# Optimization experiments

Hardware: AMD Instinct MI355X
Metric: run time of the kernel (lower is better)

The kernel has to match this reference:

```python
import jax, jax.numpy as jnp
import numpy as np

B, S, D, H, E, K, F = 8, 2048, 1024, 16, 32, 8, 1024
HD = D // H
EPS = 1e-5


def _ln(x, scale, bias):
    m = jnp.mean(x, axis=-1, keepdims=True)
    v = jnp.mean(jnp.square(x - m), axis=-1, keepdims=True)
    return (x - m) * jax.lax.rsqrt(v + EPS) * scale + bias


def setup_inputs() -> dict:
    key = jax.random.key(0)
    ks = jax.random.split(key, 14)
    w = lambda k, shp: jax.random.normal(k, shp, jnp.float32) * 0.02
    return {
        "hidden_states": jax.random.normal(ks[0], (B, S, D), jnp.float32),
        "ln1_scale": jnp.ones((D,), jnp.float32),
        "ln1_bias": jnp.zeros((D,), jnp.float32),
        "wq": w(ks[1], (D, D)), "bq": jnp.zeros((D,), jnp.float32),
        "wk": w(ks[2], (D, D)), "bk": jnp.zeros((D,), jnp.float32),
        "wv": w(ks[3], (D, D)), "bv": jnp.zeros((D,), jnp.float32),
        "ln2_scale": jnp.ones((D,), jnp.float32),
        "ln2_bias": jnp.zeros((D,), jnp.float32),
        "router_w": w(ks[4], (D, E)), "router_b": jnp.zeros((E,), jnp.float32),
        "w1": w(ks[5], (E, D, F)), "b1": jnp.zeros((E, F), jnp.float32),
        "w2": w(ks[6], (E, F, D)), "b2": jnp.zeros((E, D), jnp.float32),
    }


def reference(hidden_states, ln1_scale, ln1_bias, wq, bq, wk, bk, wv, bv,
              ln2_scale, ln2_bias, router_w, router_b, w1, b1, w2, b2):
    # --- attention sub-block (faithful to source: scores are [B,S,H,H]) ---
    x = _ln(hidden_states, ln1_scale, ln1_bias)
    q = (x @ wq + bq).reshape(B, S, H, HD)
    k = (x @ wk + bk).reshape(B, S, H, HD)
    v = (x @ wv + bv).reshape(B, S, H, HD)
    scores = jnp.einsum('bshd,bsgd->bshg', q, k) / np.sqrt(HD).astype(np.float32)
    probs = jax.nn.softmax(scores, axis=-1)
    ctx = jnp.einsum('bshg,bsgd->bshd', probs, v).reshape(B, S, D)
    h1 = hidden_states + ctx
    # --- MoE sub-block: per-token top-K of E experts ---
    x2 = _ln(h1, ln2_scale, ln2_bias)
    router_probs = jax.nn.softmax(x2 @ router_w + router_b, axis=-1)  # [B,S,E]
    top_w, top_i = jax.lax.top_k(router_probs, K)
    top_w = top_w / jnp.sum(top_w, axis=-1, keepdims=True)
    # dense per-token gate over experts (zero for unselected)
    gates = jnp.sum(jax.nn.one_hot(top_i, E, dtype=x2.dtype) * top_w[..., None], axis=-2)  # [B,S,E]
    moe = jnp.zeros_like(x2)
    for e in range(E):  # fixed small expert set; unrolled under jit
        h = jax.nn.gelu(x2 @ w1[e] + b1[e], approximate=False)
        moe = moe + gates[..., e:e + 1] * (h @ w2[e] + b2[e])
    return h1 + moe
```

## Files before the change

kernel.cpp:

```cpp
#include <hip/hip_runtime.h>
#include <hip/hip_bf16.h>
#include <stdint.h>

#define TOK 16384
#define DD  1024
#define NE  32

typedef unsigned short u16;
typedef __attribute__((ext_vector_type(8))) short short8;
typedef __attribute__((ext_vector_type(4))) float f32x4;

__device__ __forceinline__ u16 f2bf(float f) {
  unsigned int u = __float_as_uint(f);
  u += 0x7fffu + ((u >> 16) & 1u);
  return (u16)(u >> 16);
}
__device__ __forceinline__ float bf2f(u16 h) {
  return __uint_as_float(((unsigned int)h) << 16);
}
__device__ __forceinline__ void gload16(const void* g, void* l) {
  __builtin_amdgcn_global_load_lds((const __attribute__((address_space(1))) void*)g,
                                   (__attribute__((address_space(3))) void*)l, 16, 0, 0);
}

__global__ __launch_bounds__(256) void k_transpose(const float* __restrict__ src,
                                                   u16* __restrict__ dst, int R, int C) {
  __shared__ float tile[32][33];
  size_t mb = (size_t)blockIdx.z * R * C;
  int c0 = blockIdx.x * 32, r0 = blockIdx.y * 32;
  int tx = threadIdx.x, ty = threadIdx.y;
#pragma unroll
  for (int i = 0; i < 4; i++)
    tile[ty + i * 8][tx] = src[mb + (size_t)(r0 + ty + i * 8) * C + c0 + tx];
  __syncthreads();
#pragma unroll
  for (int i = 0; i < 4; i++) {
    float v = tile[tx][ty + i * 8];
    dst[mb + (size_t)(c0 + ty + i * 8) * R + r0 + tx] = f2bf(v);
  }
}

__global__ __launch_bounds__(256) void k_transpose_split(const float* __restrict__ src,
                                                         u16* __restrict__ hi,
                                                         u16* __restrict__ lo, int R, int C) {
  __shared__ float tile[32][33];
  int c0 = blockIdx.x * 32, r0 = blockIdx.y * 32;
  int tx = threadIdx.x, ty = threadIdx.y;
#pragma unroll
  for (int i = 0; i < 4; i++)
    tile[ty + i * 8][tx] = src[(size_t)(r0 + ty + i * 8) * C + c0 + tx];
  __syncthreads();
#pragma unroll
  for (int i = 0; i < 4; i++) {
    float v = tile[tx][ty + i * 8];
    u16 h = f2bf(v);
    u16 l = f2bf(v - bf2f(h));
    size_t idx = (size_t)(c0 + ty + i * 8) * R + r0 + tx;
    hi[idx] = h;
    lo[idx] = l;
  }
}

__global__ __launch_bounds__(256) void k_ln1(const float* __restrict__ x,
                                             const float* __restrict__ sc,
                                             const float* __restrict__ bi,
                                             u16* __restrict__ ohi, u16* __restrict__ olo) {
  __shared__ float red[10];
  int t = blockIdx.x, tid = threadIdx.x;
  size_t base = (size_t)t * DD + tid * 4;
  float4 v = *(const float4*)(x + base);
  float s1 = v.x + v.y + v.z + v.w;
  float s2 = v.x * v.x + v.y * v.y + v.z * v.z + v.w * v.w;
  for (int o = 1; o < 64; o <<= 1) { s1 += __shfl_xor(s1, o, 64); s2 += __shfl_xor(s2, o, 64); }
  int wid = tid >> 6;
  if ((tid & 63) == 0) { red[wid * 2] = s1; red[wid * 2 + 1] = s2; }
  __syncthreads();
  if (tid == 0) {
    float a = 0, b = 0;
    for (int i = 0; i < 4; i++) { a += red[i * 2]; b += red[i * 2 + 1]; }
    float mean = a * (1.f / DD);
    float var = b * (1.f / DD) - mean * mean;
    red[8] = mean; red[9] = rsqrtf(var + 1e-5f);
  }
  __syncthreads();
  float mean = red[8], rs = red[9];
  int e0 = tid * 4;
  float xv[4] = {v.x, v.y, v.z, v.w};
  ushort4 oh, ol;
  u16* ph = (u16*)&oh; u16* pl = (u16*)&ol;
#pragma unroll
  for (int i = 0; i < 4; i++) {
    float f = (xv[i] - mean) * rs * sc[e0 + i] + bi[e0 + i];
    u16 h = f2bf(f);
    ph[i] = h;
    pl[i] = f2bf(f - bf2f(h));
  }
  *(ushort4*)(ohi + base) = oh;
  *(ushort4*)(olo + base) = ol;
}

__global__ __launch_bounds__(256) void k_attn(
    const float* __restrict__ hidden, const float* __restrict__ qb,
    const float* __restrict__ kb, const float* __restrict__ vb,
    const float* __restrict__ ln2s, const float* __restrict__ ln2b,
    const float* __restrict__ rw, const float* __restrict__ rb,
    float* __restrict__ out, u16* __restrict__ x2b, float* __restrict__ gates) {
  __shared__ float qs[16][68], ks[16][68], vs[16][68];
  __shared__ float probs[16][17];
  __shared__ float x2s[1024];
  __shared__ float red[12];
  __shared__ float part[8][32];
  __shared__ float logits[32];
  int t = blockIdx.x, tid = threadIdx.x;
  size_t base = (size_t)t * DD + tid * 4;
  int hh = tid >> 4, dd = (tid & 15) * 4;
  {
    float4 q4 = *(const float4*)(qb + base);
    float4 k4 = *(const float4*)(kb + base);
    float4 v4 = *(const float4*)(vb + base);
    qs[hh][dd + 0] = q4.x; qs[hh][dd + 1] = q4.y; qs[hh][dd + 2] = q4.z; qs[hh][dd + 3] = q4.w;
    ks[hh][dd + 0] = k4.x; ks[hh][dd + 1] = k4.y; ks[hh][dd + 2] = k4.z; ks[hh][dd + 3] = k4.w;
    vs[hh][dd + 0] = v4.x; vs[hh][dd + 1] = v4.y; vs[hh][dd + 2] = v4.z; vs[hh][dd + 3] = v4.w;
  }
  __syncthreads();
  {
    int g = tid & 15;
    float s = 0.f;
#pragma unroll
    for (int d = 0; d < 64; d++) s += qs[hh][d] * ks[g][d];
    s *= 0.125f;
    float mx = s;
    for (int o = 1; o < 16; o <<= 1) mx = fmaxf(mx, __shfl_xor(mx, o, 16));
    float p = __expf(s - mx);
    float sm = p;
    for (int o = 1; o < 16; o <<= 1) sm += __shfl_xor(sm, o, 16);
    probs[hh][g] = p / sm;
  }
  __syncthreads();
  float c0 = 0, c1 = 0, c2 = 0, c3 = 0;
#pragma unroll
  for (int g = 0; g < 16; g++) {
    float pw = probs[hh][g];
    c0 += pw * vs[g][dd + 0]; c1 += pw * vs[g][dd + 1];
    c2 += pw * vs[g][dd + 2]; c3 += pw * vs[g][dd + 3];
  }
  float4 hv = *(const float4*)(hidden + base);
  float h0 = hv.x + c0, h1 = hv.y + c1, h2 = hv.z + c2, h3 = hv.w + c3;
  { float4 o4; o4.x = h0; o4.y = h1; o4.z = h2; o4.w = h3; *(float4*)(out + base) = o4; }
  float s1 = h0 + h1 + h2 + h3;
  float s2 = h0 * h0 + h1 * h1 + h2 * h2 + h3 * h3;
  for (int o = 1; o < 64; o <<= 1) { s1 += __shfl_xor(s1, o, 64); s2 += __shfl_xor(s2, o, 64); }
  int wid = tid >> 6;
  if ((tid & 63) == 0) { red[wid * 2] = s1; red[wid * 2 + 1] = s2; }
  __syncthreads();
  if (tid == 0) {
    float a = 0, b = 0;
    for (int i = 0; i < 4; i++) { a += red[i * 2]; b += red[i * 2 + 1]; }
    float mean = a * (1.f / DD);
    float var = b * (1.f / DD) - mean * mean;
    red[8] = mean; red[9] = rsqrtf(var + 1e-5f);
  }
  __syncthreads();
  float mean = red[8], rs = red[9];
  int e0 = tid * 4;
  float x0 = (h0 - mean) * rs * ln2s[e0 + 0] + ln2b[e0 + 0];
  float x1 = (h1 - mean) * rs * ln2s[e0 + 1] + ln2b[e0 + 1];
  float x2 = (h2 - mean) * rs * ln2s[e0 + 2] + ln2b[e0 + 2];
  float x3 = (h3 - mean) * rs * ln2s[e0 + 3] + ln2b[e0 + 3];
  ushort4 xo; xo.x = f2bf(x0); xo.y = f2bf(x1); xo.z = f2bf(x2); xo.w = f2bf(x3);
  *(ushort4*)(x2b + base) = xo;
  x2s[e0 + 0] = x0; x2s[e0 + 1] = x1; x2s[e0 + 2] = x2; x2s[e0 + 3] = x3;
  __syncthreads();
  {
    int e = tid & 31, seg = tid >> 5;
    const float* rwp = rw + (size_t)(seg * 128) * NE + e;
    float acc = 0.f;
#pragma unroll 8
    for (int i = 0; i < 128; i++) acc += x2s[seg * 128 + i] * rwp[(size_t)i * NE];
    part[seg][e] = acc;
  }
  __syncthreads();
  if (tid < 32) {
    float l = rb[tid];
#pragma unroll
    for (int s = 0; s < 8; s++) l += part[s][tid];
    logits[tid] = l;
    float mx = l;
    for (int o = 1; o < 32; o <<= 1) mx = fmaxf(mx, __shfl_xor(mx, o, 32));
    float p = __expf(l - mx);
    float sm = p;
    for (int o = 1; o < 32; o <<= 1) sm += __shfl_xor(sm, o, 32);
    p /= sm;
    bool sel = false;
#pragma unroll
    for (int rsel = 0; rsel < 8; rsel++) {
      float bv = sel ? -1.f : p;
      int bi_ = tid;
      for (int o = 1; o < 32; o <<= 1) {
        float ov = __shfl_xor(bv, o, 32);
        int oi = __shfl_xor(bi_, o, 32);
        if (ov > bv || (ov == bv && oi < bi_)) { bv = ov; bi_ = oi; }
      }
      if (tid == bi_) sel = true;
    }
    float wsel = sel ? p : 0.f;
    float ts = wsel;
    for (int o = 1; o < 32; o <<= 1) ts += __shfl_xor(ts, o, 32);
    gates[(size_t)t * 32 + tid] = sel ? (p / ts) : 0.f;
  }
}

__global__ void k_zero32(int* p) { int i = threadIdx.x; if (i < 32) p[i] = 0; }

__global__ void k_listbuild(const float* __restrict__ gates, int* __restrict__ counts,
                            int* __restrict__ lists) {
  int t = blockIdx.x * 256 + threadIdx.x;
  for (int e = 0; e < NE; e++) {
    if (gates[(size_t)t * 32 + e] > 0.f) {
      int pos = atomicAdd(&counts[e], 1);
      lists[(size_t)e * TOK + pos] = t;
    }
  }
}

__global__ void k_scan(const int* __restrict__ counts, int* __restrict__ segoff) {
  if (threadIdx.x == 0) { int s = 0; for (int e = 0; e < NE; e++) { segoff[e] = s; s += counts[e]; } }
}

__global__ __launch_bounds__(256) void k_gemm_p(
    const u16* __restrict__ Ahi, const u16* __restrict__ Alo,
    const u16* __restrict__ qkvT,
    const float* __restrict__ bq, const float* __restrict__ bk, const float* __restrict__ bv,
    float* __restrict__ Cbase) {
  constexpr int KD = 1024;
  __shared__ alignas(16) u16 As[2][2][128 * 32];
  __shared__ alignas(16) u16 Bs[2][2][128 * 32];
  const int tid = threadIdx.x;
  const int w = tid >> 6, lane = tid & 63;
  const int bm = blockIdx.x, bn = blockIdx.y, z = blockIdx.z;
  const u16* Bhi = qkvT + (size_t)z * (2u * KD * KD);
  const u16* Blo = Bhi + (size_t)KD * KD;
  const float* bias = (z == 0) ? bq : (z == 1) ? bk : bv;
  float* C = Cbase + (size_t)z * TOK * KD;

  int rowA[2], qA[2], rowB[2];
#pragma unroll
  for (int i = 0; i < 2; i++) {
    int c = (w * 2 + i) * 64 + lane;
    int r = c >> 2;
    qA[i] = c & 3;
    rowB[i] = bn * 128 + r;
    rowA[i] = bm * 128 + r;
  }

  auto stage = [&](int buf, int k0) {
#pragma unroll
    for (int i = 0; i < 2; i++) {
      size_t ga = (size_t)rowA[i] * KD + k0 + qA[i] * 8;
      size_t gb = (size_t)rowB[i] * KD + k0 + qA[i] * 8;
      int lo_off = (w * 2 + i) * 1024;
      gload16(Ahi + ga, (char*)&As[buf][0][0] + lo_off);
      gload16(Alo + ga, (char*)&As[buf][1][0] + lo_off);
      gload16(Bhi + gb, (char*)&Bs[buf][0][0] + lo_off);
      gload16(Blo + gb, (char*)&Bs[buf][1][0] + lo_off);
    }
  };

  f32x4 acc[4][4];
#pragma unroll
  for (int m = 0; m < 4; m++)
#pragma unroll
    for (int n = 0; n < 4; n++) acc[m][n] = (f32x4)0.f;

  const int wr = (w >> 1) * 64, wc = (w & 1) * 64;
  const int la = lane & 15, lk = (lane >> 4) * 8;

  stage(0, 0);
  __syncthreads();
  for (int kt = 0; kt < 32; kt++) {
    const int cur = kt & 1;
    if (kt + 1 < 32) stage(cur ^ 1, (kt + 1) * 32);
    short8 ah[4], al[4], bh[4], bl[4];
#pragma unroll
    for (int m = 0; m < 4; m++) {
      ah[m] = *(const short8*)&As[cur][0][(wr + m * 16 + la) * 32 + lk];
      al[m] = *(const short8*)&As[cur][1][(wr + m * 16 + la) * 32 + lk];
    }
#pragma unroll
    for (int n = 0; n < 4; n++) {
      bh[n] = *(const short8*)&Bs[cur][0][(wc + n * 16 + la) * 32 + lk];
      bl[n] = *(const short8*)&Bs[cur][1][(wc + n * 16 + la) * 32 + lk];
    }
#pragma unroll
    for (int m = 0; m < 4; m++)
#pragma unroll
      for (int n = 0; n < 4; n++) {
        acc[m][n] = __builtin_amdgcn_mfma_f32_16x16x32_bf16(ah[m], bh[n], acc[m][n], 0, 0, 0);
        acc[m][n] = __builtin_amdgcn_mfma_f32_16x16x32_bf16(ah[m], bl[n], acc[m][n], 0, 0, 0);
        acc[m][n] = __builtin_amdgcn_mfma_f32_16x16x32_bf16(al[m], bh[n], acc[m][n], 0, 0, 0);
      }
    __syncthreads();
  }

  const int rl4 = (lane >> 4) * 4;
#pragma unroll
  for (int m = 0; m < 4; m++) {
#pragma unroll
    for (int n = 0; n < 4; n++) {
      const int col = bn * 128 + wc + n * 16 + la;
      const float bvv = bias[col];
      f32x4 a4 = acc[m][n];
#pragma unroll
      for (int r = 0; r < 4; r++) {
        const int grow = bm * 128 + wr + m * 16 + rl4 + r;
        C[(size_t)grow * KD + col] = a4[r] + bvv;
      }
    }
  }
}

template <int MODE>
__global__ __launch_bounds__(256) void k_gemm(
    const u16* __restrict__ A, const u16* __restrict__ BT, const float* __restrict__ bias,
    u16* __restrict__ Cb, float* __restrict__ Cf,
    const int* __restrict__ lists, const int* __restrict__ counts,
    const float* __restrict__ gatesp, const int* __restrict__ segoff) {
  constexpr int KD = 1024;
  __shared__ alignas(16) u16 As[2][128 * 32];
  __shared__ alignas(16) u16 Bs[2][128 * 32];

  int e = (int)blockIdx.z;
  int count = counts[e];
  if ((int)blockIdx.x * 128 >= count) return;
  const int* list = lists + (size_t)e * TOK;
  int so = segoff[e];
  const u16* Bp = BT + (size_t)e * (KD * KD);
  const float* bp = bias + (size_t)e * KD;

  const int tid = threadIdx.x;
  const int w = tid >> 6, lane = tid & 63;
  const int bm = blockIdx.x, bn = blockIdx.y;

  int rowA[2], qA[2], rowB[2];
#pragma unroll
  for (int i = 0; i < 2; i++) {
    int c = (w * 2 + i) * 64 + lane;
    int r = c >> 2;
    qA[i] = c & 3;
    rowB[i] = bn * 128 + r;
    int rr = bm * 128 + r;
    if constexpr (MODE == 1) rowA[i] = (rr < count) ? list[rr] : 0;
    else                     rowA[i] = so + ((rr < count) ? rr : 0);
  }

  auto stage = [&](int buf, int k0) {
#pragma unroll
    for (int i = 0; i < 2; i++) {
      gload16(A + (size_t)rowA[i] * KD + k0 + qA[i] * 8,
              (char*)&As[buf][0] + (w * 2 + i) * 1024);
      gload16(Bp + (size_t)rowB[i] * KD + k0 + qA[i] * 8,
              (char*)&Bs[buf][0] + (w * 2 + i) * 1024);
    }
  };

  f32x4 acc[4][4];
#pragma unroll
  for (int m = 0; m < 4; m++)
#pragma unroll
    for (int n = 0; n < 4; n++) acc[m][n] = (f32x4)0.f;

  const int wr = (w >> 1) * 64, wc = (w & 1) * 64;
  const int la = lane & 15, lk = (lane >> 4) * 8;

  stage(0, 0);
  __syncthreads();
#pragma unroll 2
  for (int kt = 0; kt < 32; kt++) {
    const int cur = kt & 1;
    if (kt + 1 < 32) stage(cur ^ 1, (kt + 1) * 32);
    short8 af[4], bf8[4];
#pragma unroll
    for (int m = 0; m < 4; m++)
      af[m] = *(const short8*)&As[cur][(wr + m * 16 + la) * 32 + lk];
#pragma unroll
    for (int n = 0; n < 4; n++)
      bf8[n] = *(const short8*)&Bs[cur][(wc + n * 16 + la) * 32 + lk];
#pragma unroll
    for (int m = 0; m < 4; m++)
#pragma unroll
      for (int n = 0; n < 4; n++)
        acc[m][n] = __builtin_amdgcn_mfma_f32_16x16x32_bf16(af[m], bf8[n], acc[m][n], 0, 0, 0);
    __syncthreads();
  }

  const int rl4 = (lane >> 4) * 4;
#pragma unroll
  for (int m = 0; m < 4; m++) {
#pragma unroll
    for (int n = 0; n < 4; n++) {
      const int col = bn * 128 + wc + n * 16 + la;
      const float bvv = bp[col];
      f32x4 a4 = acc[m][n];
#pragma unroll
      for (int r = 0; r < 4; r++) {
        const int grow = bm * 128 + wr + m * 16 + rl4 + r;
        float v = a4[r] + bvv;
        if constexpr (MODE == 1) {
          if (grow < count) {
            float gx = 0.5f * v * (1.0f + erff(v * 0.70710678f));
            Cb[(size_t)(so + grow) * KD + col] = f2bf(gx);
          }
        } else {
          if (grow < count) {
            const int tok = list[grow];
            const float gw = gatesp[(size_t)tok * 32 + e];
            atomicAdd(Cf + (size_t)tok * KD + col, v * gw);
          }
        }
      }
    }
  }
}

extern "C" void kernel_launch(void* const* d_in, const int* in_sizes, int n_in,
                              void* d_out, int out_size, void* d_ws, size_t ws_size,
                              hipStream_t stream) {
  (void)in_sizes; (void)n_in; (void)out_size; (void)ws_size;
  const float* hidden = (const float*)d_in[0];
  const float* ln1s = (const float*)d_in[1];
  const float* ln1b = (const float*)d_in[2];
  const float* wq = (const float*)d_in[3];
  const float* bq = (const float*)d_in[4];
  const float* wk = (const float*)d_in[5];
  const float* bk = (const float*)d_in[6];
  const float* wv = (const float*)d_in[7];
  const float* bv = (const float*)d_in[8];
  const float* ln2s = (const float*)d_in[9];
  const float* ln2b = (const float*)d_in[10];
  const float* rw = (const float*)d_in[11];
  const float* rb = (const float*)d_in[12];
  const float* w1 = (const float*)d_in[13];
  const float* b1 = (const float*)d_in[14];
  const float* w2 = (const float*)d_in[15];
  const float* b2 = (const float*)d_in[16];
  float* out = (float*)d_out;

  char* wsp = (char*)d_ws;
  size_t off = 0;
  auto alloc = [&](size_t b) -> void* {
    void* p = wsp + off;
    off += (b + 255) & ~(size_t)255;
    return p;
  };
  u16* wT = (u16*)alloc((size_t)NE * DD * DD * 2);
  u16* x_hi = (u16*)alloc((size_t)TOK * DD * 2);
  float* gates = (float*)alloc((size_t)TOK * NE * 4);
  int* counts = (int*)alloc(NE * 4);
  int* segoff = (int*)alloc((NE + 1) * 4);
  int* lists = (int*)alloc((size_t)NE * TOK * 4);
  char* pool = (char*)alloc((size_t)TOK * 8 * DD * 2);
  u16* qkvT = (u16*)pool;
  u16* x_lo = (u16*)(pool + 12u * 1024 * 1024);
  float* qkv = (float*)(pool + 44u * 1024 * 1024);
  float* qbuf = qkv;
  float* kbuf = qkv + (size_t)TOK * DD;
  float* vbuf = qkv + 2 * (size_t)TOK * DD;
  u16* h_buf = (u16*)pool;

  dim3 tb32(32, 8, 1);
  k_zero32<<<1, 64, 0, stream>>>(counts);
  k_transpose_split<<<dim3(32, 32, 1), tb32, 0, stream>>>(wq, qkvT, qkvT + (size_t)DD * DD, DD, DD);
  k_transpose_split<<<dim3(32, 32, 1), tb32, 0, stream>>>(wk, qkvT + 2 * (size_t)DD * DD, qkvT + 3 * (size_t)DD * DD, DD, DD);
  k_transpose_split<<<dim3(32, 32, 1), tb32, 0, stream>>>(wv, qkvT + 4 * (size_t)DD * DD, qkvT + 5 * (size_t)DD * DD, DD, DD);
  k_transpose<<<dim3(32, 32, NE), tb32, 0, stream>>>(w1, wT, DD, DD);
  k_ln1<<<TOK, 256, 0, stream>>>(hidden, ln1s, ln1b, x_hi, x_lo);
  k_gemm_p<<<dim3(128, 8, 3), 256, 0, stream>>>(x_hi, x_lo, qkvT, bq, bk, bv, qkv);
  k_attn<<<TOK, 256, 0, stream>>>(hidden, qbuf, kbuf, vbuf, ln2s, ln2b, rw, rb, out, x_hi, gates);
  k_listbuild<<<TOK / 256, 256, 0, stream>>>(gates, counts, lists);
  k_scan<<<1, 32, 0, stream>>>(counts, segoff);
  k_gemm<1><<<dim3(128, 8, NE), 256, 0, stream>>>(x_hi, wT, b1, h_buf, nullptr, lists, counts, nullptr, segoff);
  k_transpose<<<dim3(32, 32, NE), tb32, 0, stream>>>(w2, wT, DD, DD);
  k_gemm<2><<<dim3(128, 8, NE), 256, 0, stream>>>(h_buf, wT, b2, nullptr, out, lists, counts, gates, segoff);
}
```

Before: 2.532 ms.

## Replace atomic scatter-add in second MoE GEMM with bf16 staging and gather

```diff
diff --git a/kernel.cpp b/kernel.cpp
--- a/kernel.cpp
+++ b/kernel.cpp
@@ -110,7 +110,6 @@
   __shared__ float x2s[1024];
   __shared__ float red[12];
   __shared__ float part[8][32];
-  __shared__ float logits[32];
   int t = blockIdx.x, tid = threadIdx.x;
   size_t base = (size_t)t * DD + tid * 4;
   int hh = tid >> 4, dd = (tid & 15) * 4;
@@ -184,7 +183,6 @@
     float l = rb[tid];
 #pragma unroll
     for (int s = 0; s < 8; s++) l += part[s][tid];
-    logits[tid] = l;
     float mx = l;
     for (int o = 1; o < 32; o <<= 1) mx = fmaxf(mx, __shfl_xor(mx, o, 32));
     float p = __expf(l - mx);
@@ -213,12 +211,18 @@
 __global__ void k_zero32(int* p) { int i = threadIdx.x; if (i < 32) p[i] = 0; }
 
 __global__ void k_listbuild(const float* __restrict__ gates, int* __restrict__ counts,
-                            int* __restrict__ lists) {
+                            int* __restrict__ lists, int* __restrict__ slots,
+                            float* __restrict__ gsel) {
   int t = blockIdx.x * 256 + threadIdx.x;
+  int j = 0;
   for (int e = 0; e < NE; e++) {
-    if (gates[(size_t)t * 32 + e] > 0.f) {
+    float g = gates[(size_t)t * 32 + e];
+    if (g > 0.f && j < 8) {
       int pos = atomicAdd(&counts[e], 1);
       lists[(size_t)e * TOK + pos] = t;
+      slots[t * 8 + j] = (e << 14) | pos;
+      gsel[t * 8 + j] = g;
+      j++;
     }
   }
 }
@@ -319,12 +323,10 @@
   }
 }
 
-template <int MODE>
-__global__ __launch_bounds__(256) void k_gemm(
+__global__ __launch_bounds__(256) void k_gemm1(
     const u16* __restrict__ A, const u16* __restrict__ BT, const float* __restrict__ bias,
-    u16* __restrict__ Cb, float* __restrict__ Cf,
-    const int* __restrict__ lists, const int* __restrict__ counts,
-    const float* __restrict__ gatesp, const int* __restrict__ segoff) {
+    u16* __restrict__ Cb, const int* __restrict__ lists, const int* __restrict__ counts,
+    const int* __restrict__ segoff) {
   constexpr int KD = 1024;
   __shared__ alignas(16) u16 As[2][128 * 32];
   __shared__ alignas(16) u16 Bs[2][128 * 32];
@@ -349,8 +351,7 @@
     qA[i] = c & 3;
     rowB[i] = bn * 128 + r;
     int rr = bm * 128 + r;
-    if constexpr (MODE == 1) rowA[i] = (rr < count) ? list[rr] : 0;
-    else                     rowA[i] = so + ((rr < count) ? rr : 0);
+    rowA[i] = (rr < count) ? list[rr] : 0;
   }
 
   auto stage = [&](int buf, int k0) {
@@ -404,28 +405,132 @@
 #pragma unroll
       for (int r = 0; r < 4; r++) {
         const int grow = bm * 128 + wr + m * 16 + rl4 + r;
-        float v = a4[r] + bvv;
-        if constexpr (MODE == 1) {
-          if (grow < count) {
-            float gx = 0.5f * v * (1.0f + erff(v * 0.70710678f));
-            Cb[(size_t)(so + grow) * KD + col] = f2bf(gx);
-          }
-        } else {
-          if (grow < count) {
-            const int tok = list[grow];
-            const float gw = gatesp[(size_t)tok * 32 + e];
-            atomicAdd(Cf + (size_t)tok * KD + col, v * gw);
-          }
+        if (grow < count) {
+          float v = a4[r] + bvv;
+          float gx = 0.5f * v * (1.0f + erff(v * 0.70710678f));
+          Cb[(size_t)(so + grow) * KD + col] = f2bf(gx);
         }
       }
     }
   }
+}
+
+__global__ __launch_bounds__(256) void k_gemm2(
+    const u16* __restrict__ A, const u16* __restrict__ BT, const float* __restrict__ bias,
+    u16* __restrict__ out2, const int* __restrict__ counts, const int* __restrict__ segoff,
+    int col0, int C) {
+  constexpr int KD = 1024;
+  __shared__ alignas(16) u16 As[2][128 * 32];
+  __shared__ alignas(16) u16 Bs[2][128 * 32];
+
+  int e = (int)blockIdx.z;
+  int count = counts[e];
+  if ((int)blockIdx.x * 128 >= count) return;
+  int so = segoff[e];
+  const u16* Bp = BT + (size_t)e * (KD * KD);
+  const float* bp = bias + (size_t)e * KD;
+
+  const int tid = threadIdx.x;
+  const int w = tid >> 6, lane = tid & 63;
+  const int bm = blockIdx.x, bn = blockIdx.y;
+
+  int rowA[2], qA[2], rowB[2];
+#pragma unroll
+  for (int i = 0; i < 2; i++) {
+    int c = (w * 2 + i) * 64 + lane;
+    int r = c >> 2;
+    qA[i] = c & 3;
+    rowB[i] = col0 + bn * 128 + r;
+    int rr = bm * 128 + r;
+    rowA[i] = so + ((rr < count) ? rr : 0);
+  }
+
+  auto stage = [&](int buf, int k0) {
+#pragma unroll
+    for (int i = 0; i < 2; i++) {
+      gload16(A + (size_t)rowA[i] * KD + k0 + qA[i] * 8,
+              (char*)&As[buf][0] + (w * 2 + i) * 1024);
+      gload16(Bp + (size_t)rowB[i] * KD + k0 + qA[i] * 8,
+              (char*)&Bs[buf][0] + (w * 2 + i) * 1024);
+    }
+  };
+
+  f32x4 acc[4][4];
+#pragma unroll
+  for (int m = 0; m < 4; m++)
+#pragma unroll
+    for (int n = 0; n < 4; n++) acc[m][n] = (f32x4)0.f;
+
+  const int wr = (w >> 1) * 64, wc = (w & 1) * 64;
+  const int la = lane & 15, lk = (lane >> 4) * 8;
+
+  stage(0, 0);
+  __syncthreads();
+#pragma unroll 2
+  for (int kt = 0; kt < 32; kt++) {
+    const int cur = kt & 1;
+    if (kt + 1 < 32) stage(cur ^ 1, (kt + 1) * 32);
+    short8 af[4], bf8[4];
+#pragma unroll
+    for (int m = 0; m < 4; m++)
+      af[m] = *(const short8*)&As[cur][(wr + m * 16 + la) * 32 + lk];
+#pragma unroll
+    for (int n = 0; n < 4; n++)
+      bf8[n] = *(const short8*)&Bs[cur][(wc + n * 16 + la) * 32 + lk];
+#pragma unroll
+    for (int m = 0; m < 4; m++)
+#pragma unroll
+      for (int n = 0; n < 4; n++)
+        acc[m][n] = __builtin_amdgcn_mfma_f32_16x16x32_bf16(af[m], bf8[n], acc[m][n], 0, 0, 0);
+    __syncthreads();
+  }
+
+  const int rl4 = (lane >> 4) * 4;
+#pragma unroll
+  for (int m = 0; m < 4; m++) {
+#pragma unroll
+    for (int n = 0; n < 4; n++) {
+      const int lcol = bn * 128 + wc + n * 16 + la;
+      const float bvv = bp[col0 + lcol];
+      f32x4 a4 = acc[m][n];
+#pragma unroll
+      for (int r = 0; r < 4; r++) {
+        const int grow = bm * 128 + wr + m * 16 + rl4 + r;
+        if (grow < count)
+          out2[(size_t)(so + grow) * C + lcol] = f2bf(a4[r] + bvv);
+      }
+    }
+  }
+}
+
+__global__ __launch_bounds__(256) void k_gather(
+    const float* __restrict__ gsel, const int* __restrict__ slots,
+    const int* __restrict__ segoff, const u16* __restrict__ out2,
+    float* __restrict__ out, int col0, int C, int cshift) {
+  int tid4 = threadIdx.x * 4;
+  int tpb = 1024 >> cshift;
+  int t = blockIdx.x * tpb + (tid4 >> cshift);
+  int c4 = tid4 & (C - 1);
+  float a0 = 0, a1 = 0, a2 = 0, a3 = 0;
+#pragma unroll
+  for (int j = 0; j < 8; j++) {
+    int s = slots[t * 8 + j];
+    float g = gsel[t * 8 + j];
+    int seg = segoff[s >> 14] + (s & 16383);
+    ushort4 v4 = *(const ushort4*)(out2 + (size_t)seg * C + c4);
+    a0 += g * bf2f(v4.x); a1 += g * bf2f(v4.y);
+    a2 += g * bf2f(v4.z); a3 += g * bf2f(v4.w);
+  }
+  size_t ob = (size_t)t * DD + col0 + c4;
+  float4 o = *(const float4*)(out + ob);
+  o.x += a0; o.y += a1; o.z += a2; o.w += a3;
+  *(float4*)(out + ob) = o;
 }
 
 extern "C" void kernel_launch(void* const* d_in, const int* in_sizes, int n_in,
                               void* d_out, int out_size, void* d_ws, size_t ws_size,
                               hipStream_t stream) {
-  (void)in_sizes; (void)n_in; (void)out_size; (void)ws_size;
+  (void)in_sizes; (void)n_in; (void)out_size;
   const float* hidden = (const float*)d_in[0];
   const float* ln1s = (const float*)d_in[1];
   const float* ln1b = (const float*)d_in[2];
@@ -453,10 +558,12 @@
     return p;
   };
   u16* wT = (u16*)alloc((size_t)NE * DD * DD * 2);
+  int* slots = (int*)alloc((size_t)TOK * 8 * 4);
+  float* gsel = (float*)alloc((size_t)TOK * 8 * 4);
+  int* counts = (int*)alloc(NE * 4);
+  int* segoff = (int*)alloc((NE + 1) * 4);
   u16* x_hi = (u16*)alloc((size_t)TOK * DD * 2);
   float* gates = (float*)alloc((size_t)TOK * NE * 4);
-  int* counts = (int*)alloc(NE * 4);
-  int* segoff = (int*)alloc((NE + 1) * 4);
   int* lists = (int*)alloc((size_t)NE * TOK * 4);
   char* pool = (char*)alloc((size_t)TOK * 8 * DD * 2);
   u16* qkvT = (u16*)pool;
@@ -467,6 +574,16 @@
   float* vbuf = qkv + 2 * (size_t)TOK * DD;
   u16* h_buf = (u16*)pool;
 
+  const size_t ROWS = (size_t)TOK * 8;
+  size_t extra = (ws_size > off) ? ws_size - off : 0;
+  int C;
+  u16* out2;
+  if (extra >= ROWS * 1024 * 2 + 1024) { C = 1024; out2 = (u16*)alloc(ROWS * 1024 * 2); }
+  else if (extra >= ROWS * 512 * 2 + 1024) { C = 512; out2 = (u16*)alloc(ROWS * 512 * 2); }
+  else if (extra >= ROWS * 256 * 2 + 1024) { C = 256; out2 = (u16*)alloc(ROWS * 256 * 2); }
+  else { C = 128; out2 = (u16*)x_hi; }
+  int cshift = 31 - __builtin_clz((unsigned)C);
+
   dim3 tb32(32, 8, 1);
   k_zero32<<<1, 64, 0, stream>>>(counts);
   k_transpose_split<<<dim3(32, 32, 1), tb32, 0, stream>>>(wq, qkvT, qkvT + (size_t)DD * DD, DD, DD);
@@ -476,9 +593,12 @@
   k_ln1<<<TOK, 256, 0, stream>>>(hidden, ln1s, ln1b, x_hi, x_lo);
   k_gemm_p<<<dim3(128, 8, 3), 256, 0, stream>>>(x_hi, x_lo, qkvT, bq, bk, bv, qkv);
   k_attn<<<TOK, 256, 0, stream>>>(hidden, qbuf, kbuf, vbuf, ln2s, ln2b, rw, rb, out, x_hi, gates);
-  k_listbuild<<<TOK / 256, 256, 0, stream>>>(gates, counts, lists);
+  k_listbuild<<<TOK / 256, 256, 0, stream>>>(gates, counts, lists, slots, gsel);
   k_scan<<<1, 32, 0, stream>>>(counts, segoff);
-  k_gemm<1><<<dim3(128, 8, NE), 256, 0, stream>>>(x_hi, wT, b1, h_buf, nullptr, lists, counts, nullptr, segoff);
+  k_gemm1<<<dim3(128, 8, NE), 256, 0, stream>>>(x_hi, wT, b1, h_buf, lists, counts, segoff);
   k_transpose<<<dim3(32, 32, NE), tb32, 0, stream>>>(w2, wT, DD, DD);
-  k_gemm<2><<<dim3(128, 8, NE), 256, 0, stream>>>(h_buf, wT, b2, nullptr, out, lists, counts, gates, segoff);
-}
+  for (int c0 = 0; c0 < DD; c0 += C) {
+    k_gemm2<<<dim3(128, C / 128, NE), 256, 0, stream>>>(h_buf, wT, b2, out2, counts, segoff, c0, C);
+    k_gather<<<TOK >> (10 - cshift), 256, 0, stream>>>(gsel, slots, segoff, out2, out, c0, C, cshift);
+  }
+}
```

After: 2.037 ms. -19.5%, faster.
